# Optimization experiments

Hardware: AMD Instinct MI355X
Metric: run time of the kernel (lower is better)

The kernel has to match this reference:

```python
import jax, jax.numpy as jnp
import numpy as np

LAMBDA_TEMP = 20.0
GAMMA = 20.0
MARGIN = 0.05
EPS = 1e-8

B, K, M, D = 128, 256, 8, 128


def _unit(x, axis=-1):
    return x / jnp.linalg.norm(x, axis=axis, keepdims=True)


def setup_inputs() -> dict:
    key = jax.random.key(0)
    k1, k2, k3 = jax.random.split(key, 3)
    v_proj = _unit(jax.random.normal(k1, (B, K, D), dtype=jnp.float32))
    prototypes = _unit(jax.random.normal(k2, (K, M, D), dtype=jnp.float32))
    concept_labels = jax.random.randint(k3, (B, K), 0, 2, dtype=jnp.int64)
    return {"v_proj": v_proj, "concept_labels": concept_labels, "prototypes": prototypes}


def reference(v_proj, concept_labels, prototypes):
    # all-pairs prototype similarities: query vector (b,k) vs prototypes of concept c
    # sims: (B, K, C, M)
    sims = jnp.einsum('bkd,cmd->bkcm', v_proj, prototypes)
    # Eq.6: soft assignment over the M prototypes of each concept
    q = jax.nn.softmax(GAMMA * sims, axis=-1)
    # Eq.7-8: weighted similarity sim_c(v)  -> (B, K, C)
    sim = jnp.sum(q * sims, axis=-1)
    # positive similarity: concept k queried against its own prototypes, plus margin
    sim_pos = jnp.einsum('bkk->bk', sim) + MARGIN  # (B, K)
    # Eq.9: -log( exp(lam*sim_pos) / (sum_c exp(lam*sim_c) + eps) )
    denom = jnp.sum(jnp.exp(LAMBDA_TEMP * sim), axis=-1) + EPS  # (B, K)
    loss_bk = jnp.log(denom) - LAMBDA_TEMP * sim_pos  # (B, K)
    mask = (concept_labels == 1).astype(loss_bk.dtype)
    num_pos = jnp.sum(mask)
    total = jnp.sum(loss_bk * mask)
    return jnp.where(num_pos > 0, total / num_pos, total)
```

## Files before the change

### kernel.cpp

```cpp
#include <hip/hip_runtime.h>

#define LT      20.0f
#define LN2     0.69314718055994531f
#define C2EXP   28.853900817779268f
#define CHUNKS  16
#define NBLK    1024

typedef _Float16 half8  __attribute__((ext_vector_type(8)));
typedef float    f32x16 __attribute__((ext_vector_type(16)));

#if __has_builtin(__builtin_amdgcn_exp2f)
#define EXP2F(x) __builtin_amdgcn_exp2f(x)
#else
#define EXP2F(x) __expf(0.69314718055994531f * (x))
#endif

#define GLD16(gp, lp) __builtin_amdgcn_global_load_lds( \
    (const __attribute__((address_space(1))) void*)(gp), \
    (__attribute__((address_space(3))) void*)(lp), 16, 0, 0)


__global__ __launch_bounds__(1024)
void mpcl_prep_compact(const float* __restrict__ P,
                       const int*   __restrict__ labels,
                       _Float16* __restrict__ Pw,
                       int* __restrict__ ridx, int* __restrict__ npos)
{
    __shared__ int wcnt[512];
    __shared__ int wsum[8];
    __shared__ int sbase[512];
    __shared__ int tot;

    if (blockIdx.x < 32) {
        int t    = blockIdx.x * 1024 + threadIdx.x;
        int gcol = t >> 4;
        int dblk = t & 15;
        const float* src = P + ((size_t)gcol << 7) + dblk * 8;
        float4 x0 = *(const float4*)src;
        float4 x1 = *(const float4*)(src + 4);

        int ch = gcol >> 7, col = gcol & 127;
        int g  = col >> 5,  col5 = col & 31;
        int cl = col5 >> 3, p = col5 & 7;
        int a  = (p & 3) | ((cl & 1) << 2) | ((cl >> 1) << 3) | ((p >> 2) << 4);
        int hi = dblk & 1, s = dblk >> 1;
        int l  = (hi << 5) | a;
        int slot = ch * 2048 + (g * 8 + s) * 64 + l;

        half8 hv;
        hv[0] = (_Float16)(C2EXP * x0.x); hv[1] = (_Float16)(C2EXP * x0.y);
        hv[2] = (_Float16)(C2EXP * x0.z); hv[3] = (_Float16)(C2EXP * x0.w);
        hv[4] = (_Float16)(C2EXP * x1.x); hv[5] = (_Float16)(C2EXP * x1.y);
        hv[6] = (_Float16)(C2EXP * x1.z); hv[7] = (_Float16)(C2EXP * x1.w);
        *(half8*)(Pw + (size_t)slot * 8) = hv;
    } else {
        const int tid = threadIdx.x, lane = tid & 63, w = tid >> 6;
        int lab[32];
#pragma unroll
        for (int i = 0; i < 32; ++i) lab[i] = labels[i * 1024 + tid];
#pragma unroll
        for (int i = 0; i < 32; ++i) {
            unsigned long long m = __ballot(lab[i] == 1);
            if (lane == 0) wcnt[i * 16 + w] = __popcll(m);
        }
        __syncthreads();

        int v = 0, orig = 0;
        if (tid < 512) { v = wcnt[tid]; orig = v; }
#pragma unroll
        for (int off = 1; off < 64; off <<= 1) {
            int t2 = __shfl_up(v, off);
            if (lane >= off) v += t2;
        }
        if (lane == 63 && w < 8) wsum[w] = v;
        __syncthreads();
        if (tid == 0) {
            int acc = 0;
#pragma unroll
            for (int i = 0; i < 8; ++i) { int t2 = wsum[i]; wsum[i] = acc; acc += t2; }
            tot = acc; npos[0] = acc;
        }
        __syncthreads();
        if (tid < 512) sbase[tid] = v - orig + wsum[w];
        __syncthreads();

#pragma unroll
        for (int i = 0; i < 32; ++i) {
            unsigned long long m = __ballot(lab[i] == 1);
            int pos = sbase[i * 16 + w] + __popcll(m & ((1ull << lane) - 1));
            if (lab[i] == 1) ridx[pos] = i * 1024 + tid;
        }
        for (int j = tot + tid; j < 32768; j += 1024) ridx[j] = 0;
    }
}

__global__ __attribute__((amdgpu_flat_work_group_size(256, 256),
                          amdgpu_waves_per_eu(4, 4)))
void mpcl_main(const float* __restrict__ V,
               const _Float16* __restrict__ Pw,
               const int* __restrict__ ridx,
               const int* __restrict__ npos,
               float* __restrict__ part)
{
    __shared__ __align__(16) _Float16 Pst[2][16384];
    __shared__ float sh_denom[32];
    __shared__ float sh_simpos[32];

    const int np = *npos;
    const int rowbase = blockIdx.x * 32;
    if (rowbase >= np) return;

    const int tid = threadIdx.x;
    const int l   = tid & 63;
    const int w   = tid >> 6;
    const int a   = l & 31;
    const int hi  = l >> 5;

    if (tid < 32) sh_denom[tid] = 0.0f;

    const int pos   = rowbase + a;
    const int myrow = ridx[pos < np ? pos : np - 1];
    const int rowk  = myrow & 255;

    half8 vh[8];
    {
        const float* vr = V + ((size_t)myrow << 7) + hi * 8;
#pragma unroll
        for (int s = 0; s < 8; ++s) {
            float4 x0 = *(const float4*)(vr + s * 16);
            float4 x1 = *(const float4*)(vr + s * 16 + 4);
            vh[s][0] = (_Float16)x0.x; vh[s][1] = (_Float16)x0.y;
            vh[s][2] = (_Float16)x0.z; vh[s][3] = (_Float16)x0.w;
            vh[s][4] = (_Float16)x1.x; vh[s][5] = (_Float16)x1.y;
            vh[s][6] = (_Float16)x1.z; vh[s][7] = (_Float16)x1.w;
        }
    }
    __syncthreads();

    const _Float16* gbase = Pw + (size_t)(w * 512 + l) * 8;

#define STAGE(CH, B) do {                                       \
    const _Float16* g_ = gbase + (size_t)(CH) * 16384;          \
    _Float16* l_ = &Pst[B][w * 4096];                           \
    GLD16(g_,        l_);        GLD16(g_ +  512, l_ +  512);   \
    GLD16(g_ + 1024, l_ + 1024); GLD16(g_ + 1536, l_ + 1536);   \
    GLD16(g_ + 2048, l_ + 2048); GLD16(g_ + 2560, l_ + 2560);   \
    GLD16(g_ + 3072, l_ + 3072); GLD16(g_ + 3584, l_ + 3584);   \
} while (0)

    STAGE(0, 0);
    STAGE(1, 1);

    float dn = 0.f;

#define SOFT8(y0,y1,y2,y3,y4,y5,y6,y7, CONCEPT) do {                        \
    float e0=EXP2F(y0), e1=EXP2F(y1), e2=EXP2F(y2), e3=EXP2F(y3);           \
    float e4=EXP2F(y4), e5=EXP2F(y5), e6=EXP2F(y6), e7=EXP2F(y7);           \
    float es = ((e0+e1)+(e2+e3)) + ((e4+e5)+(e6+e7));                       \
    float ss = fmaf(e0,y0, fmaf(e1,y1, fmaf(e2,y2, e3*y3)))                 \
             + fmaf(e4,y4, fmaf(e5,y5, fmaf(e6,y6, e7*y7)));                \
    float simY = __fdividef(ss, es);                   \
    dn += EXP2F(simY);                                                      \
    if ((CONCEPT) == rowk) sh_simpos[a] = simY; \
} while (0)

#pragma unroll 1
    for (int ch = 0; ch < CHUNKS; ++ch) {
        if (ch < CHUNKS - 1) asm volatile("s_waitcnt vmcnt(8)" ::: "memory");
        else                 asm volatile("s_waitcnt vmcnt(0)" ::: "memory");

        const _Float16* bs = &Pst[ch & 1][w * 4096];
        f32x16 acA = {0.f,0.f,0.f,0.f,0.f,0.f,0.f,0.f,0.f,0.f,0.f,0.f,0.f,0.f,0.f,0.f};
        f32x16 acB = {0.f,0.f,0.f,0.f,0.f,0.f,0.f,0.f,0.f,0.f,0.f,0.f,0.f,0.f,0.f,0.f};
        {
            half8 p0 = *(const half8*)&bs[l * 8];
            half8 p4 = *(const half8*)&bs[l * 8 + 4 * 512];
            acA = __builtin_amdgcn_mfma_f32_32x32x16_f16(p0, vh[0], acA, 0, 0, 0);
            acB = __builtin_amdgcn_mfma_f32_32x32x16_f16(p4, vh[4], acB, 0, 0, 0);
            half8 p1 = *(const half8*)&bs[l * 8 + 1 * 512];
            half8 p5 = *(const half8*)&bs[l * 8 + 5 * 512];
            acA = __builtin_amdgcn_mfma_f32_32x32x16_f16(p1, vh[1], acA, 0, 0, 0);
            acB = __builtin_amdgcn_mfma_f32_32x32x16_f16(p5, vh[5], acB, 0, 0, 0);
            half8 p2 = *(const half8*)&bs[l * 8 + 2 * 512];
            half8 p6 = *(const half8*)&bs[l * 8 + 6 * 512];
            acA = __builtin_amdgcn_mfma_f32_32x32x16_f16(p2, vh[2], acA, 0, 0, 0);
            acB = __builtin_amdgcn_mfma_f32_32x32x16_f16(p6, vh[6], acB, 0, 0, 0);
            half8 p3 = *(const half8*)&bs[l * 8 + 3 * 512];
            half8 p7 = *(const half8*)&bs[l * 8 + 7 * 512];
            acA = __builtin_amdgcn_mfma_f32_32x32x16_f16(p3, vh[3], acA, 0, 0, 0);
            acB = __builtin_amdgcn_mfma_f32_32x32x16_f16(p7, vh[7], acB, 0, 0, 0);
        }
        asm volatile("s_waitcnt lgkmcnt(0)" ::: "memory");
        if (ch + 2 < CHUNKS) STAGE(ch + 2, ch & 1);

        f32x16 acc = acA + acB;
        const int cb = (ch << 4) + (w << 2) + hi;
        SOFT8(acc[0], acc[1], acc[2],  acc[3],  acc[8],  acc[9],  acc[10], acc[11], cb);
        SOFT8(acc[4], acc[5], acc[6],  acc[7],  acc[12], acc[13], acc[14], acc[15], cb + 2);
    }

    {
        float t = dn;
        t += __shfl_xor(t, 32);
        if (hi == 0)
            atomicAdd(&sh_denom[a], t);
    }
    __syncthreads();

    if (w == 0) {
        float s = 0.f, cc = 0.f;
        if (l < 32 && rowbase + l < np) {
            s  = logf(sh_denom[l] + 1e-8f) - LN2 * sh_simpos[l] - 1.0f;
            cc = 1.0f;
        }
#pragma unroll
        for (int off = 32; off >= 1; off >>= 1) {
            s  += __shfl_down(s, off);
            cc += __shfl_down(cc, off);
        }
        if (l == 0) {
            part[2 * blockIdx.x]     = s;
            part[2 * blockIdx.x + 1] = cc;
        }
    }
}

__global__ __launch_bounds__(512)
void mpcl_finish(const float* __restrict__ part, const int* __restrict__ npos,
                 float* __restrict__ out)
{
    __shared__ float sh[16];
    const int tid  = threadIdx.x;
    const int lane = tid & 63;
    const int w    = tid >> 6;
    const int nact = (*npos + 31) >> 5;

    float s = 0.f, cc = 0.f;
    for (int i = tid; i < nact; i += 512) {
        s  += part[2 * i];
        cc += part[2 * i + 1];
    }
#pragma unroll
    for (int off = 32; off >= 1; off >>= 1) {
        s  += __shfl_down(s, off);
        cc += __shfl_down(cc, off);
    }
    if (lane == 0) { sh[w] = s; sh[8 + w] = cc; }
    __syncthreads();
    if (tid == 0) {
        float ts = 0.f, tc = 0.f;
#pragma unroll
        for (int i = 0; i < 8; ++i) { ts += sh[i]; tc += sh[8 + i]; }
        out[0] = (tc > 0.0f) ? (ts / tc) : ts;
    }
}

extern "C" void kernel_launch(void* const* d_in, const int* in_sizes, int n_in,
                              void* d_out, int out_size, void* d_ws, size_t ws_size,
                              hipStream_t stream)
{
    const float* V      = (const float*)d_in[0];
    const int*   labels = (const int*)d_in[1];
    const float* P      = (const float*)d_in[2];
    float* out = (float*)d_out;

    int*      npos = (int*)d_ws;
    float*    part = (float*)((char*)d_ws + 256);
    int*      ridx = (int*)((char*)d_ws + 16384);
    _Float16* Pw   = (_Float16*)((char*)d_ws + 147456);

    mpcl_prep_compact<<<33, 1024, 0, stream>>>(P, labels, Pw, ridx, npos);
    mpcl_main<<<NBLK, 256, 0, stream>>>(V, Pw, ridx, npos, part);
    mpcl_finish<<<1, 512, 0, stream>>>(part, npos, out);
}
```

Before: 93.97 us.

## Split concept chunks across two wave groups in 512-thread blocks

The main kernel now runs 8 waves per block instead of 4. The two halves of the block each process 8 of the 16 prototype chunks for the same 32 rows, which halves the serial chunk loop per wave. The LDS staging is reorganised into per-wave half-chunk double buffers, so each wave issues 4 global-to-LDS loads per half-chunk and waits at finer granularity. The cost is duplicated V loads and conversions per row, more LDS and wave pressure per block, and partial denominators from both wave groups merged through shared atomics.

```diff
diff --git a/kernel.cpp b/kernel.cpp
--- a/kernel.cpp
+++ b/kernel.cpp
@@ -94,7 +94,7 @@
     }
 }
 
-__global__ __attribute__((amdgpu_flat_work_group_size(256, 256),
+__global__ __attribute__((amdgpu_flat_work_group_size(512, 512),
                           amdgpu_waves_per_eu(4, 4)))
 void mpcl_main(const float* __restrict__ V,
                const _Float16* __restrict__ Pw,
@@ -102,7 +102,7 @@
                const int* __restrict__ npos,
                float* __restrict__ part)
 {
-    __shared__ __align__(16) _Float16 Pst[2][16384];
+    __shared__ __align__(16) _Float16 Pst[8 * 4096];
     __shared__ float sh_denom[32];
     __shared__ float sh_simpos[32];
 
@@ -113,6 +113,8 @@
     const int tid = threadIdx.x;
     const int l   = tid & 63;
     const int w   = tid >> 6;
+    const int g   = w & 3;
+    const int kh  = w >> 2;
     const int a   = l & 31;
     const int hi  = l >> 5;
 
@@ -137,19 +139,19 @@
     }
     __syncthreads();
 
-    const _Float16* gbase = Pw + (size_t)(w * 512 + l) * 8;
-
-#define STAGE(CH, B) do {                                       \
-    const _Float16* g_ = gbase + (size_t)(CH) * 16384;          \
-    _Float16* l_ = &Pst[B][w * 4096];                           \
-    GLD16(g_,        l_);        GLD16(g_ +  512, l_ +  512);   \
-    GLD16(g_ + 1024, l_ + 1024); GLD16(g_ + 1536, l_ + 1536);   \
-    GLD16(g_ + 2048, l_ + 2048); GLD16(g_ + 2560, l_ + 2560);   \
-    GLD16(g_ + 3072, l_ + 3072); GLD16(g_ + 3584, l_ + 3584);   \
+    const _Float16* gbase = Pw + (size_t)g * 4096 + (size_t)l * 8;
+    _Float16* lbase = &Pst[w * 4096];
+
+#define STAGEH(CH, HF, B) do {                                        \
+    const _Float16* g_ = gbase + (size_t)(CH) * 16384 + (HF) * 2048;  \
+    _Float16* l_ = lbase + (B) * 2048;                                \
+    GLD16(g_,        l_);        GLD16(g_ +  512, l_ +  512);         \
+    GLD16(g_ + 1024, l_ + 1024); GLD16(g_ + 1536, l_ + 1536);         \
 } while (0)
 
-    STAGE(0, 0);
-    STAGE(1, 1);
+    const int ch0 = kh * 8;
+    STAGEH(ch0, 0, 0);
+    STAGEH(ch0, 1, 1);
 
     float dn = 0.f;
 
@@ -161,40 +163,49 @@
              + fmaf(e4,y4, fmaf(e5,y5, fmaf(e6,y6, e7*y7)));                \
     float simY = __fdividef(ss, es);                   \
     dn += EXP2F(simY);                                                      \
-    if ((CONCEPT) == rowk) sh_simpos[a] = simY; \
+    if ((CONCEPT) == rowk) sh_simpos[a] = simY;      \
 } while (0)
 
 #pragma unroll 1
-    for (int ch = 0; ch < CHUNKS; ++ch) {
-        if (ch < CHUNKS - 1) asm volatile("s_waitcnt vmcnt(8)" ::: "memory");
-        else                 asm volatile("s_waitcnt vmcnt(0)" ::: "memory");
-
-        const _Float16* bs = &Pst[ch & 1][w * 4096];
+    for (int i = 0; i < 8; ++i) {
+        const int ch = ch0 + i;
+
         f32x16 acA = {0.f,0.f,0.f,0.f,0.f,0.f,0.f,0.f,0.f,0.f,0.f,0.f,0.f,0.f,0.f,0.f};
         f32x16 acB = {0.f,0.f,0.f,0.f,0.f,0.f,0.f,0.f,0.f,0.f,0.f,0.f,0.f,0.f,0.f,0.f};
+
+        asm volatile("s_waitcnt vmcnt(4)" ::: "memory");
         {
+            const _Float16* bs = lbase;
             half8 p0 = *(const half8*)&bs[l * 8];
-            half8 p4 = *(const half8*)&bs[l * 8 + 4 * 512];
+            half8 p1 = *(const half8*)&bs[l * 8 + 512];
             acA = __builtin_amdgcn_mfma_f32_32x32x16_f16(p0, vh[0], acA, 0, 0, 0);
+            half8 p2 = *(const half8*)&bs[l * 8 + 1024];
+            acA = __builtin_amdgcn_mfma_f32_32x32x16_f16(p1, vh[1], acA, 0, 0, 0);
+            half8 p3 = *(const half8*)&bs[l * 8 + 1536];
+            acA = __builtin_amdgcn_mfma_f32_32x32x16_f16(p2, vh[2], acA, 0, 0, 0);
+            acA = __builtin_amdgcn_mfma_f32_32x32x16_f16(p3, vh[3], acA, 0, 0, 0);
+        }
+        asm volatile("s_waitcnt lgkmcnt(0)" ::: "memory");
+        if (i + 1 < 8) STAGEH(ch + 1, 0, 0);
+
+        if (i < 7) asm volatile("s_waitcnt vmcnt(4)" ::: "memory");
+        else       asm volatile("s_waitcnt vmcnt(0)" ::: "memory");
+        {
+            const _Float16* bs = lbase + 2048;
+            half8 p4 = *(const half8*)&bs[l * 8];
+            half8 p5 = *(const half8*)&bs[l * 8 + 512];
             acB = __builtin_amdgcn_mfma_f32_32x32x16_f16(p4, vh[4], acB, 0, 0, 0);
-            half8 p1 = *(const half8*)&bs[l * 8 + 1 * 512];
-            half8 p5 = *(const half8*)&bs[l * 8 + 5 * 512];
-            acA = __builtin_amdgcn_mfma_f32_32x32x16_f16(p1, vh[1], acA, 0, 0, 0);
+            half8 p6 = *(const half8*)&bs[l * 8 + 1024];
             acB = __builtin_amdgcn_mfma_f32_32x32x16_f16(p5, vh[5], acB, 0, 0, 0);
-            half8 p2 = *(const half8*)&bs[l * 8 + 2 * 512];
-            half8 p6 = *(const half8*)&bs[l * 8 + 6 * 512];
-            acA = __builtin_amdgcn_mfma_f32_32x32x16_f16(p2, vh[2], acA, 0, 0, 0);
+            half8 p7 = *(const half8*)&bs[l * 8 + 1536];
             acB = __builtin_amdgcn_mfma_f32_32x32x16_f16(p6, vh[6], acB, 0, 0, 0);
-            half8 p3 = *(const half8*)&bs[l * 8 + 3 * 512];
-            half8 p7 = *(const half8*)&bs[l * 8 + 7 * 512];
-            acA = __builtin_amdgcn_mfma_f32_32x32x16_f16(p3, vh[3], acA, 0, 0, 0);
             acB = __builtin_amdgcn_mfma_f32_32x32x16_f16(p7, vh[7], acB, 0, 0, 0);
         }
         asm volatile("s_waitcnt lgkmcnt(0)" ::: "memory");
-        if (ch + 2 < CHUNKS) STAGE(ch + 2, ch & 1);
+        if (i + 1 < 8) STAGEH(ch + 1, 1, 1);
 
         f32x16 acc = acA + acB;
-        const int cb = (ch << 4) + (w << 2) + hi;
+        const int cb = (ch << 4) + (g << 2) + hi;
         SOFT8(acc[0], acc[1], acc[2],  acc[3],  acc[8],  acc[9],  acc[10], acc[11], cb);
         SOFT8(acc[4], acc[5], acc[6],  acc[7],  acc[12], acc[13], acc[14], acc[15], cb + 2);
     }
@@ -270,6 +281,6 @@
     _Float16* Pw   = (_Float16*)((char*)d_ws + 147456);
 
     mpcl_prep_compact<<<33, 1024, 0, stream>>>(P, labels, Pw, ridx, npos);
-    mpcl_main<<<NBLK, 256, 0, stream>>>(V, Pw, ridx, npos, part);
+    mpcl_main<<<NBLK, 512, 0, stream>>>(V, Pw, ridx, npos, part);
     mpcl_finish<<<1, 512, 0, stream>>>(part, npos, out);
 }
```

After: 94.50 us. About the same (+0.6%).
